# Optimization experiments

Measured on AMD Instinct MI355X. Metric: run time of the kernel, lower is better.

The kernel has to match this reference:

```python
import jax, jax.numpy as jnp
import numpy as np

B, CZ, E, V, H, W = 256, 512, 512, 4096, 16, 16  # batch, z_channels, embed_dim, vocab, latent HxW


def setup_inputs() -> dict:
    key = jax.random.key(0)
    k0, k1, k2, k3 = jax.random.split(key, 4)
    x = jax.random.normal(k0, (B, CZ, H, W), jnp.float32)          # encoder feature map
    pre_w = jax.random.normal(k1, (E, CZ), jnp.float32) * 0.02     # 1x1 pre_quant_conv weight
    pre_b = jnp.zeros((E,), jnp.float32)
    emb = jax.random.uniform(k2, (V, E), jnp.float32, -1.0 / V, 1.0 / V)  # codebook, uniform init as in module
    post_w = jax.random.normal(k3, (CZ, E), jnp.float32) * 0.02    # 1x1 post_quant_conv weight
    post_b = jnp.zeros((CZ,), jnp.float32)
    return dict(x=x, pre_w=pre_w, pre_b=pre_b, emb=emb, post_w=post_w, post_b=post_b)


def reference(x, pre_w, pre_b, emb, post_w, post_b):
    # pre_quant_conv: 1x1 Conv2d(CZ -> E)
    z = jnp.einsum('bchw,ec->behw', x, pre_w) + pre_b[None, :, None, None]
    b, e, h, w = z.shape
    # flatten spatial: (b h w, e)
    zf = z.transpose(0, 2, 3, 1).reshape(-1, e)
    # expanded squared-distance to codebook: ||z||^2 + ||c||^2 - 2 z.c
    dist = (jnp.sum(zf * zf, axis=1, keepdims=True)
            + jnp.sum(emb * emb, axis=1)
            - 2.0 * zf @ emb.T)                                    # [bhw, V]
    tokens = jnp.argmin(dist, axis=-1)                             # [bhw] int
    z_q = emb[tokens].reshape(b, h, w, e).transpose(0, 3, 1, 2)    # gather -> [b,e,h,w]
    # straight-through estimator
    dec_in = z + jax.lax.stop_gradient(z_q - z)
    # post_quant_conv: 1x1 Conv2d(E -> CZ)
    rec = jnp.einsum('behw,ce->bchw', dec_in, post_w) + post_b[None, :, None, None]
    return z, z_q, rec
```

## Files before the change

### kernel.cpp

```cpp
#include <hip/hip_runtime.h>
#include <hip/hip_bf16.h>

typedef unsigned short u16;
typedef unsigned int   u32;
typedef unsigned long long u64;

using short8 = __attribute__((ext_vector_type(8))) short;
using f32x4  = __attribute__((ext_vector_type(4))) float;
using u16x8  = __attribute__((ext_vector_type(8))) unsigned short;

#define AS_GLOBAL __attribute__((address_space(1)))
#define AS_LDS    __attribute__((address_space(3)))

__device__ __forceinline__ u16 f2b(float x){
  u32 u = __float_as_uint(x);
  u32 r = (u + 0x7FFFu + ((u >> 16) & 1u)) >> 16;
  return (u16)r;
}
__device__ __forceinline__ float b2f(u16 h){ return __uint_as_float(((u32)h) << 16); }

__device__ __forceinline__ void gload16(u16* l, const u16* g){
  __builtin_amdgcn_global_load_lds((const AS_GLOBAL u32*)g, (AS_LDS u32*)l, 16, 0, 0);
}

__device__ __forceinline__ u64 umin64(u64 a, u64 b){ return a < b ? a : b; }

__device__ __forceinline__ u64 shfl_xor_u64(u64 v, int m){
  u32 lo = __shfl_xor((u32)v, m, 64);
  u32 hi = __shfl_xor((u32)(v >> 32), m, 64);
  return ((u64)hi << 32) | lo;
}

__device__ __forceinline__ void waitv4(){ asm volatile("s_waitcnt vmcnt(4)" ::: "memory"); }
__device__ __forceinline__ void waitv0(){ asm volatile("s_waitcnt vmcnt(0)" ::: "memory"); }

__global__ void k_cvt(const float* __restrict__ w, u16* __restrict__ d, int n){
  int i = blockIdx.x * 256 + threadIdx.x;
  if (i < n) d[i] = f2b(w[i]);
}

__global__ void k_cnorm(const float* __restrict__ emb, float* __restrict__ cnorm){
  int v = blockIdx.x, lane = threadIdx.x;
  const float* r = emb + (size_t)v * 512;
  float s = 0.f;
  #pragma unroll
  for (int i = 0; i < 8; ++i){ float x = r[lane + i * 64]; s += x * x; }
  #pragma unroll
  for (int off = 32; off; off >>= 1) s += __shfl_down(s, off, 64);
  if (lane == 0) cnorm[v] = s;
}

__global__ void k_tcvt(const float* __restrict__ src, u16* __restrict__ d){
  __shared__ float t[64][65];
  const int bid = blockIdx.x;
  const int b  = bid >> 5;
  const int rb = (bid >> 2) & 7;
  const int cb = bid & 3;
  const float* s = src + ((size_t)b * 512 + (size_t)rb * 64) * 256 + cb * 64;
  const int tid = threadIdx.x;
  #pragma unroll
  for (int j = 0; j < 4; ++j){
    int fl = j * 256 + tid;
    int r = fl >> 4, c4 = (fl & 15) * 4;
    float4 v = *(const float4*)(s + (size_t)r * 256 + c4);
    t[r][c4 + 0] = v.x; t[r][c4 + 1] = v.y; t[r][c4 + 2] = v.z; t[r][c4 + 3] = v.w;
  }
  __syncthreads();
  u16* o = d + ((size_t)b * 256 + (size_t)cb * 64) * 512 + rb * 64;
  #pragma unroll
  for (int j = 0; j < 2; ++j){
    int fl = j * 256 + tid;
    int c = fl >> 3, r8 = (fl & 7) * 8;
    u16x8 hv;
    #pragma unroll
    for (int i = 0; i < 8; ++i) hv[i] = f2b(t[r8 + i][c]);
    *(u16x8*)(o + (size_t)c * 512 + r8) = hv;
  }
}

__global__ void k_zq(const u64* __restrict__ keys, const float* __restrict__ emb, float* __restrict__ zq){
  int sidx = blockIdx.x * 64 + threadIdx.x;
  int b = sidx >> 8, s = sidx & 255;
  int v = (int)(u32)keys[sidx];
  const float4* er = (const float4*)(emb + (size_t)v * 512);
  float* o = zq + (size_t)b * 512 * 256 + s;
  #pragma unroll 4
  for (int e4 = 0; e4 < 128; ++e4){
    float4 vv = er[e4];
    o[(size_t)(e4 * 4 + 0) * 256] = vv.x;
    o[(size_t)(e4 * 4 + 1) * 256] = vv.y;
    o[(size_t)(e4 * 4 + 2) * 256] = vv.z;
    o[(size_t)(e4 * 4 + 3) * 256] = vv.w;
  }
}

template<int MODE>
__global__ __launch_bounds__(256, 4) void k_gemm(
    const u16* __restrict__ Ah,
    const u16* __restrict__ Bh,
    const u64* __restrict__ gkeys,
    const float* __restrict__ bias,
    const float* __restrict__ cnorm,
    float* __restrict__ Cout,
    u64* __restrict__ okeys,
    int M, int mtbits)
{
  constexpr int K = 512;
  __shared__ __align__(16) u16 sA[128 * 64];
  __shared__ __align__(16) u16 sB[128 * 64];

  const int tid  = threadIdx.x;
  const int lane = tid & 63;
  const int wid  = tid >> 6;
  const int wm = wid >> 1, wn = wid & 1;

  const int nwg = gridDim.x;
  const int chunk = nwg >> 3;
  const int pb = blockIdx.x;
  const int bid = (pb & 7) * chunk + (pb >> 3);

  const int mt = bid & ((1 << mtbits) - 1);
  const int nt = (bid >> mtbits) & 1;
  const int b  = bid >> (mtbits + 1);
  const int m0 = mt * 128;
  const int n0 = nt * 128;
  const int bbase = b * 256;

  const u16* ga[4];
  const u16* gb[4];
  int ldso[4];
  #pragma unroll
  for (int i = 0; i < 4; ++i){
    int e = i * 256 + tid;
    int r = e >> 3;
    int sl = (e & 7) ^ (r & 7);
    ldso[i] = e * 8;
    ga[i] = Ah + (size_t)(m0 + r) * K + sl * 8;
    size_t brow;
    if (MODE == 2) brow = (size_t)(u32)gkeys[bbase + n0 + r];
    else           brow = (size_t)(bbase + n0 + r);
    gb[i] = Bh + brow * K + sl * 8;
  }

  const f32x4 zero4 = {0.f, 0.f, 0.f, 0.f};
  f32x4 acc[4][4];
  #pragma unroll
  for (int i = 0; i < 4; ++i)
    #pragma unroll
    for (int j = 0; j < 4; ++j) acc[i][j] = zero4;

  int aoff[2][4], boff[2][4];
  #pragma unroll
  for (int ks = 0; ks < 2; ++ks)
    #pragma unroll
    for (int f = 0; f < 4; ++f){
      int rA = wm * 64 + f * 16 + (lane & 15);
      aoff[ks][f] = rA * 64 + (((ks * 4 + (lane >> 4)) ^ (rA & 7)) * 8);
      int rB = wn * 64 + f * 16 + (lane & 15);
      boff[ks][f] = rB * 64 + (((ks * 4 + (lane >> 4)) ^ (rB & 7)) * 8);
    }

  for (int kt = 0; kt < 8; ++kt){
    const int k0 = kt * 64;
    #pragma unroll
    for (int i = 0; i < 4; ++i){
      gload16(&sA[ldso[i]], ga[i] + k0);
      gload16(&sB[ldso[i]], gb[i] + k0);
    }
    __syncthreads();
    #pragma unroll
    for (int ks = 0; ks < 2; ++ks){
      short8 ah[4], bh[4];
      #pragma unroll
      for (int f = 0; f < 4; ++f){
        ah[f] = *(const short8*)&sA[aoff[ks][f]];
        bh[f] = *(const short8*)&sB[boff[ks][f]];
      }
      #pragma unroll
      for (int fm = 0; fm < 4; ++fm)
        #pragma unroll
        for (int fn = 0; fn < 4; ++fn)
          acc[fm][fn] = __builtin_amdgcn_mfma_f32_16x16x32_bf16(ah[fm], bh[fn], acc[fm][fn], 0, 0, 0);
    }
    __syncthreads();
  }

  if (MODE != 1){
    const int row0 = m0 + wm * 64;
    const int col  = n0 + wn * 64 + (lane & 15);
    float* Cb = Cout + (size_t)b * M * 256;
    #pragma unroll
    for (int fm = 0; fm < 4; ++fm){
      #pragma unroll
      for (int j = 0; j < 4; ++j){
        int row = row0 + fm * 16 + (lane >> 4) * 4 + j;
        float bi = bias[row];
        #pragma unroll
        for (int fn = 0; fn < 4; ++fn)
          Cb[(size_t)row * 256 + col + fn * 16] = acc[fm][fn][j] + bi;
      }
    }
  }
}

__global__ __launch_bounds__(512, 2) void k_gemm2(
    const u16* __restrict__ Ah,
    const u16* __restrict__ Bh,
    const float* __restrict__ cnorm,
    u64* __restrict__ okeys)
{
  __shared__ __align__(16) u16 lds[2][32768];

  const int tid  = threadIdx.x;
  const int lane = tid & 63;
  const int wid  = tid >> 6;
  const int wm   = wid >> 2;
  const int wn   = wid & 3;

  const int nwg = gridDim.x;
  const int chunk = nwg >> 3;
  const int pb  = blockIdx.x;
  const int bid = (pb & 7) * chunk + (pb >> 3);
  const int mt = bid & 15;
  const int b  = bid >> 4;
  const int m0 = mt * 256;
  const int bbase = b * 256;

  const int l8 = lane >> 3;
  const int sl = (lane & 7) ^ l8;
  const int arb = (wid < 4) ? wid * 16 : 128 + (wid - 4) * 16;
  const int brb = (wid >> 1) * 64 + (wid & 1) * 16;

  const u16* srcA0 = Ah + (size_t)(m0 + arb + l8) * 512 + sl * 8;
  const u16* srcA1 = srcA0 + 8 * 512;
  const u16* srcB0 = Bh + (size_t)(bbase + brb + l8) * 512 + sl * 8;
  const u16* srcB1 = srcB0 + 8 * 512;
  const int dA0 = arb * 64 + lane * 8;
  const int dA1 = dA0 + 512;
  const int dB0 = 16384 + brb * 64 + lane * 8;
  const int dB1 = dB0 + 512;

#define STG_AFML(p, kk) { gload16(&lds[p][dA0], srcA0 + (kk)); gload16(&lds[p][dA1], srcA1 + (kk)); }
#define STG_AFMH(p, kk) { gload16(&lds[p][dA0 + 4096], srcA0 + 32768 + (kk)); gload16(&lds[p][dA1 + 4096], srcA1 + 32768 + (kk)); }
#define STG_BFNL(p, kk) { gload16(&lds[p][dB0], srcB0 + (kk)); gload16(&lds[p][dB1], srcB1 + (kk)); }
#define STG_BFNH(p, kk) { gload16(&lds[p][dB0 + 2048], srcB0 + 16384 + (kk)); gload16(&lds[p][dB1 + 2048], srcB1 + 16384 + (kk)); }

  int aoff[2][8], boff[2][4];
  #pragma unroll
  for (int ks = 0; ks < 2; ++ks){
    #pragma unroll
    for (int f = 0; f < 8; ++f){
      int rA = wm * 128 + f * 16 + (lane & 15);
      aoff[ks][f] = rA * 64 + (((ks * 4 + (lane >> 4)) ^ (rA & 7)) * 8);
    }
    #pragma unroll
    for (int f = 0; f < 4; ++f){
      int rB = wn * 64 + f * 16 + (lane & 15);
      boff[ks][f] = 16384 + rB * 64 + (((ks * 4 + (lane >> 4)) ^ (rB & 7)) * 8);
    }
  }

  const f32x4 zero4 = {0.f, 0.f, 0.f, 0.f};
  f32x4 acc[8][4];
  #pragma unroll
  for (int i = 0; i < 8; ++i)
    #pragma unroll
    for (int j = 0; j < 4; ++j) acc[i][j] = zero4;

  STG_AFML(0, 0) STG_AFMH(0, 0) STG_BFNL(0, 0) STG_BFNH(0, 0)
  STG_AFML(1, 64) STG_BFNH(1, 64)
  waitv4();
  __builtin_amdgcn_s_barrier();
  __builtin_amdgcn_sched_barrier(0);

  for (int t = 0; t < 8; ++t){
    const int bc = t & 1;
    const int bn = bc ^ 1;
    const u16* cb = &lds[bc][0];
    const int kn1 = (t + 1) * 64, kn2 = (t + 2) * 64;
    short8 ah[4][2], bh[2][2];

    if (t < 7) STG_AFMH(bn, kn1)
    #pragma unroll
    for (int f = 0; f < 4; ++f){ ah[f][0] = *(const short8*)&cb[aoff[0][f]]; ah[f][1] = *(const short8*)&cb[aoff[1][f]]; }
    #pragma unroll
    for (int f = 0; f < 2; ++f){ bh[f][0] = *(const short8*)&cb[boff[0][f]]; bh[f][1] = *(const short8*)&cb[boff[1][f]]; }
    __builtin_amdgcn_s_setprio(1);
    #pragma unroll
    for (int fm = 0; fm < 4; ++fm)
      #pragma unroll
      for (int fn = 0; fn < 2; ++fn){
        acc[fm][fn] = __builtin_amdgcn_mfma_f32_16x16x32_bf16(ah[fm][0], bh[fn][0], acc[fm][fn], 0, 0, 0);
        acc[fm][fn] = __builtin_amdgcn_mfma_f32_16x16x32_bf16(ah[fm][1], bh[fn][1], acc[fm][fn], 0, 0, 0);
      }
    __builtin_amdgcn_s_setprio(0);
    __builtin_amdgcn_sched_barrier(0);
    __builtin_amdgcn_s_barrier();
    __builtin_amdgcn_sched_barrier(0);

    if (t < 7) STG_BFNL(bn, kn1)
    #pragma unroll
    for (int f = 0; f < 2; ++f){ bh[f][0] = *(const short8*)&cb[boff[0][2 + f]]; bh[f][1] = *(const short8*)&cb[boff[1][2 + f]]; }
    __builtin_amdgcn_s_setprio(1);
    #pragma unroll
    for (int fm = 0; fm < 4; ++fm)
      #pragma unroll
      for (int fn = 0; fn < 2; ++fn){
        acc[fm][2 + fn] = __builtin_amdgcn_mfma_f32_16x16x32_bf16(ah[fm][0], bh[fn][0], acc[fm][2 + fn], 0, 0, 0);
        acc[fm][2 + fn] = __builtin_amdgcn_mfma_f32_16x16x32_bf16(ah[fm][1], bh[fn][1], acc[fm][2 + fn], 0, 0, 0);
      }
    __builtin_amdgcn_s_setprio(0);
    __builtin_amdgcn_sched_barrier(0);
    __builtin_amdgcn_s_barrier();
    __builtin_amdgcn_sched_barrier(0);

    if (t < 6) STG_AFML(bc, kn2)
    #pragma unroll
    for (int f = 0; f < 4; ++f){ ah[f][0] = *(const short8*)&cb[aoff[0][4 + f]]; ah[f][1] = *(const short8*)&cb[aoff[1][4 + f]]; }
    __builtin_amdgcn_s_setprio(1);
    #pragma unroll
    for (int fm = 0; fm < 4; ++fm)
      #pragma unroll
      for (int fn = 0; fn < 2; ++fn){
        acc[4 + fm][2 + fn] = __builtin_amdgcn_mfma_f32_16x16x32_bf16(ah[fm][0], bh[fn][0], acc[4 + fm][2 + fn], 0, 0, 0);
        acc[4 + fm][2 + fn] = __builtin_amdgcn_mfma_f32_16x16x32_bf16(ah[fm][1], bh[fn][1], acc[4 + fm][2 + fn], 0, 0, 0);
      }
    __builtin_amdgcn_s_setprio(0);
    __builtin_amdgcn_sched_barrier(0);
    __builtin_amdgcn_s_barrier();
    __builtin_amdgcn_sched_barrier(0);

    if (t < 6) STG_BFNH(bc, kn2)
    #pragma unroll
    for (int f = 0; f < 2; ++f){ bh[f][0] = *(const short8*)&cb[boff[0][f]]; bh[f][1] = *(const short8*)&cb[boff[1][f]]; }
    __builtin_amdgcn_s_setprio(1);
    #pragma unroll
    for (int fm = 0; fm < 4; ++fm)
      #pragma unroll
      for (int fn = 0; fn < 2; ++fn){
        acc[4 + fm][fn] = __builtin_amdgcn_mfma_f32_16x16x32_bf16(ah[fm][0], bh[fn][0], acc[4 + fm][fn], 0, 0, 0);
        acc[4 + fm][fn] = __builtin_amdgcn_mfma_f32_16x16x32_bf16(ah[fm][1], bh[fn][1], acc[4 + fm][fn], 0, 0, 0);
      }
    __builtin_amdgcn_s_setprio(0);
    __builtin_amdgcn_sched_barrier(0);
    if (t < 6) waitv4(); else if (t == 6) waitv0();
    __builtin_amdgcn_s_barrier();
    __builtin_amdgcn_sched_barrier(0);
  }

  __syncthreads();
  u64 best[4];
  #pragma unroll
  for (int fn = 0; fn < 4; ++fn){
    u64 bk = ~0ull;
    #pragma unroll
    for (int fm = 0; fm < 8; ++fm){
      #pragma unroll
      for (int j = 0; j < 4; ++j){
        int v = m0 + wm * 128 + fm * 16 + (lane >> 4) * 4 + j;
        float sc = cnorm[v] - 2.0f * acc[fm][fn][j];
        u32 o = __float_as_uint(sc);
        o = (o & 0x80000000u) ? ~o : (o | 0x80000000u);
        bk = umin64(bk, ((u64)o << 32) | (u32)v);
      }
    }
    bk = umin64(bk, shfl_xor_u64(bk, 16));
    bk = umin64(bk, shfl_xor_u64(bk, 32));
    best[fn] = bk;
  }
  u64* kbuf = (u64*)&lds[0][0];
  if (lane < 16){
    #pragma unroll
    for (int fn = 0; fn < 4; ++fn)
      kbuf[wm * 256 + wn * 64 + fn * 16 + lane] = best[fn];
  }
  __syncthreads();
  if (tid < 256){
    u64 k2 = umin64(kbuf[tid], kbuf[256 + tid]);
    atomicMin((unsigned long long*)(okeys + bbase + tid), (unsigned long long)k2);
  }
#undef STG_AFML
#undef STG_AFMH
#undef STG_BFNL
#undef STG_BFNH
}

extern "C" void kernel_launch(void* const* d_in, const int* in_sizes, int n_in,
                              void* d_out, int out_size, void* d_ws, size_t ws_size,
                              hipStream_t stream){
  const float* x      = (const float*)d_in[0];
  const float* pre_w  = (const float*)d_in[1];
  const float* pre_b  = (const float*)d_in[2];
  const float* emb    = (const float*)d_in[3];
  const float* post_w = (const float*)d_in[4];
  const float* post_b = (const float*)d_in[5];

  float* z_out   = (float*)d_out;
  float* zq_out  = z_out + 33554432;
  float* rec_out = z_out + 67108864;

  char* w = (char*)d_ws;
  u16* prew_b  = (u16*)(w);
  u16* postw_b = (u16*)(w + 524288);
  u16* emb_b   = (u16*)(w + 1048576);
  float* cnorm = (float*)(w + 5242880);
  u64* keys    = (u64*)(w + 5259264);
  u16* xb      = (u16*)(w + 5783552);
  u16* zb = xb;

  k_cvt  <<<1024, 256, 0, stream>>>(pre_w, prew_b, 262144);
  k_cvt  <<<1024, 256, 0, stream>>>(post_w, postw_b, 262144);
  k_cvt  <<<8192, 256, 0, stream>>>(emb, emb_b, 2097152);
  k_cnorm<<<4096, 64, 0, stream>>>(emb, cnorm);
  hipMemsetAsync(keys, 0xFF, 65536 * sizeof(u64), stream);

  k_tcvt<<<8192, 256, 0, stream>>>(x, xb);

  k_gemm<0><<<256 * 2 * 4, 256, 0, stream>>>(prew_b, xb,
      nullptr, pre_b, nullptr, z_out, nullptr, 512, 2);

  k_tcvt<<<8192, 256, 0, stream>>>(z_out, zb);

  k_gemm2<<<256 * 16, 512, 0, stream>>>(emb_b, zb, cnorm, keys);

  k_zq<<<1024, 64, 0, stream>>>(keys, emb, zq_out);

  k_gemm<2><<<256 * 2 * 4, 256, 0, stream>>>(postw_b, emb_b,
      keys, post_b, nullptr, rec_out, nullptr, 512, 2);
}
```

Measured before the change: 548.9 us.

## Make distance GEMM persistent per batch, looping codebook tiles with in-register argmin

The codebook-distance kernel now launches one workgroup per batch image, 256 in total, instead of one per (batch, codebook tile) pair. Each workgroup loops over all 16 codebook tiles with a continuous double-buffered K pipeline, keeps the running argmin in registers, and caches the codebook norms in LDS. This removes the global atomicMin and the keys memset, and cuts per-workgroup setup overhead. The cost is a 256-workgroup grid with one 512-thread block per batch, which may underfill the GPU's compute units, plus a larger LDS footprint that lowers occupancy.

```diff
diff --git a/kernel.cpp b/kernel.cpp
--- a/kernel.cpp
+++ b/kernel.cpp
@@ -30,9 +30,6 @@
   u32 hi = __shfl_xor((u32)(v >> 32), m, 64);
   return ((u64)hi << 32) | lo;
 }
-
-__device__ __forceinline__ void waitv4(){ asm volatile("s_waitcnt vmcnt(4)" ::: "memory"); }
-__device__ __forceinline__ void waitv0(){ asm volatile("s_waitcnt vmcnt(0)" ::: "memory"); }
 
 __global__ void k_cvt(const float* __restrict__ w, u16* __restrict__ d, int n){
   int i = blockIdx.x * 256 + threadIdx.x;
@@ -100,9 +97,7 @@
     const u16* __restrict__ Bh,
     const u64* __restrict__ gkeys,
     const float* __restrict__ bias,
-    const float* __restrict__ cnorm,
     float* __restrict__ Cout,
-    u64* __restrict__ okeys,
     int M, int mtbits)
 {
   constexpr int K = 512;
@@ -185,20 +180,18 @@
     __syncthreads();
   }
 
-  if (MODE != 1){
-    const int row0 = m0 + wm * 64;
-    const int col  = n0 + wn * 64 + (lane & 15);
-    float* Cb = Cout + (size_t)b * M * 256;
-    #pragma unroll
-    for (int fm = 0; fm < 4; ++fm){
-      #pragma unroll
-      for (int j = 0; j < 4; ++j){
-        int row = row0 + fm * 16 + (lane >> 4) * 4 + j;
-        float bi = bias[row];
-        #pragma unroll
-        for (int fn = 0; fn < 4; ++fn)
-          Cb[(size_t)row * 256 + col + fn * 16] = acc[fm][fn][j] + bi;
-      }
+  const int row0 = m0 + wm * 64;
+  const int col  = n0 + wn * 64 + (lane & 15);
+  float* Cb = Cout + (size_t)b * M * 256;
+  #pragma unroll
+  for (int fm = 0; fm < 4; ++fm){
+    #pragma unroll
+    for (int j = 0; j < 4; ++j){
+      int row = row0 + fm * 16 + (lane >> 4) * 4 + j;
+      float bi = bias[row];
+      #pragma unroll
+      for (int fn = 0; fn < 4; ++fn)
+        Cb[(size_t)row * 256 + col + fn * 16] = acc[fm][fn][j] + bi;
     }
   }
 }
@@ -209,41 +202,40 @@
     const float* __restrict__ cnorm,
     u64* __restrict__ okeys)
 {
-  __shared__ __align__(16) u16 lds[2][32768];
+  __shared__ __align__(16) u16 lds[75776];
 
   const int tid  = threadIdx.x;
   const int lane = tid & 63;
   const int wid  = tid >> 6;
   const int wm   = wid >> 2;
   const int wn   = wid & 3;
-
-  const int nwg = gridDim.x;
-  const int chunk = nwg >> 3;
-  const int pb  = blockIdx.x;
-  const int bid = (pb & 7) * chunk + (pb >> 3);
-  const int mt = bid & 15;
-  const int b  = bid >> 4;
-  const int m0 = mt * 256;
+  const int b    = blockIdx.x;
   const int bbase = b * 256;
+
+  float* cn = (float*)&lds[65536];
+  {
+    const float4* c4 = (const float4*)cnorm;
+    float4 a0 = c4[tid], a1 = c4[tid + 512];
+    ((float4*)cn)[tid] = a0; ((float4*)cn)[tid + 512] = a1;
+  }
+  __syncthreads();
 
   const int l8 = lane >> 3;
   const int sl = (lane & 7) ^ l8;
   const int arb = (wid < 4) ? wid * 16 : 128 + (wid - 4) * 16;
   const int brb = (wid >> 1) * 64 + (wid & 1) * 16;
-
-  const u16* srcA0 = Ah + (size_t)(m0 + arb + l8) * 512 + sl * 8;
-  const u16* srcA1 = srcA0 + 8 * 512;
-  const u16* srcB0 = Bh + (size_t)(bbase + brb + l8) * 512 + sl * 8;
-  const u16* srcB1 = srcB0 + 8 * 512;
-  const int dA0 = arb * 64 + lane * 8;
-  const int dA1 = dA0 + 512;
-  const int dB0 = 16384 + brb * 64 + lane * 8;
-  const int dB1 = dB0 + 512;
-
-#define STG_AFML(p, kk) { gload16(&lds[p][dA0], srcA0 + (kk)); gload16(&lds[p][dA1], srcA1 + (kk)); }
-#define STG_AFMH(p, kk) { gload16(&lds[p][dA0 + 4096], srcA0 + 32768 + (kk)); gload16(&lds[p][dA1 + 4096], srcA1 + 32768 + (kk)); }
-#define STG_BFNL(p, kk) { gload16(&lds[p][dB0], srcB0 + (kk)); gload16(&lds[p][dB1], srcB1 + (kk)); }
-#define STG_BFNH(p, kk) { gload16(&lds[p][dB0 + 2048], srcB0 + 16384 + (kk)); gload16(&lds[p][dB1 + 2048], srcB1 + 16384 + (kk)); }
+  const size_t aS = (size_t)(arb + l8) * 512 + sl * 8;
+  const size_t bS = (size_t)(bbase + brb + l8) * 512 + sl * 8;
+  const int dA = arb * 64 + lane * 8;
+  const int dB = 16384 + brb * 64 + lane * 8;
+
+#define STG_AFML(tp) if ((tp) < 128){ const u16* s_ = Ah + (size_t)((tp) >> 3) * 131072 + aS + ((tp) & 7) * 64; u16* d_ = &lds[((tp) & 1) * 32768 + dA]; gload16(d_, s_); gload16(d_ + 512, s_ + 4096); }
+#define STG_AFMH(tp) if ((tp) < 128){ const u16* s_ = Ah + (size_t)((tp) >> 3) * 131072 + aS + 32768 + ((tp) & 7) * 64; u16* d_ = &lds[((tp) & 1) * 32768 + dA + 4096]; gload16(d_, s_); gload16(d_ + 512, s_ + 4096); }
+#define STG_BFNL(tp) if ((tp) < 128){ const u16* s_ = Bh + bS + ((tp) & 7) * 64; u16* d_ = &lds[((tp) & 1) * 32768 + dB]; gload16(d_, s_); gload16(d_ + 512, s_ + 4096); }
+#define STG_BFNH(tp) if ((tp) < 128){ const u16* s_ = Bh + bS + 16384 + ((tp) & 7) * 64; u16* d_ = &lds[((tp) & 1) * 32768 + dB + 2048]; gload16(d_, s_); gload16(d_ + 512, s_ + 4096); }
+
+#define PH_WAIT(tau_) { if ((tau_) < 126){ asm volatile("s_waitcnt vmcnt(10)" ::: "memory"); } else { asm volatile("s_waitcnt vmcnt(0)" ::: "memory"); } \
+  __builtin_amdgcn_s_barrier(); __builtin_amdgcn_sched_barrier(0); }
 
   int aoff[2][8], boff[2][4];
   #pragma unroll
@@ -267,122 +259,123 @@
     #pragma unroll
     for (int j = 0; j < 4; ++j) acc[i][j] = zero4;
 
-  STG_AFML(0, 0) STG_AFMH(0, 0) STG_BFNL(0, 0) STG_BFNH(0, 0)
-  STG_AFML(1, 64) STG_BFNH(1, 64)
-  waitv4();
-  __builtin_amdgcn_s_barrier();
-  __builtin_amdgcn_sched_barrier(0);
-
-  for (int t = 0; t < 8; ++t){
-    const int bc = t & 1;
-    const int bn = bc ^ 1;
-    const u16* cb = &lds[bc][0];
-    const int kn1 = (t + 1) * 64, kn2 = (t + 2) * 64;
-    short8 ah[4][2], bh[2][2];
-
-    if (t < 7) STG_AFMH(bn, kn1)
-    #pragma unroll
-    for (int f = 0; f < 4; ++f){ ah[f][0] = *(const short8*)&cb[aoff[0][f]]; ah[f][1] = *(const short8*)&cb[aoff[1][f]]; }
-    #pragma unroll
-    for (int f = 0; f < 2; ++f){ bh[f][0] = *(const short8*)&cb[boff[0][f]]; bh[f][1] = *(const short8*)&cb[boff[1][f]]; }
-    __builtin_amdgcn_s_setprio(1);
-    #pragma unroll
-    for (int fm = 0; fm < 4; ++fm)
-      #pragma unroll
-      for (int fn = 0; fn < 2; ++fn){
-        acc[fm][fn] = __builtin_amdgcn_mfma_f32_16x16x32_bf16(ah[fm][0], bh[fn][0], acc[fm][fn], 0, 0, 0);
-        acc[fm][fn] = __builtin_amdgcn_mfma_f32_16x16x32_bf16(ah[fm][1], bh[fn][1], acc[fm][fn], 0, 0, 0);
+  u64 best[4];
+  #pragma unroll
+  for (int i = 0; i < 4; ++i) best[i] = ~0ull;
+
+  short8 ah[4][2], bhL[2][2], bhH[2][2];
+
+  STG_AFML(0) STG_BFNL(0) STG_BFNH(0) STG_AFMH(0)
+  STG_AFML(1) STG_BFNL(1) STG_BFNH(1)
+
+  for (int mt = 0; mt < 16; ++mt){
+    #pragma unroll 2
+    for (int kt = 0; kt < 8; ++kt){
+      const int tau = mt * 8 + kt;
+      const int bb_ = (tau & 1) * 32768;
+
+      PH_WAIT(tau);
+      STG_AFMH(tau + 1)
+      #pragma unroll
+      for (int f = 0; f < 4; ++f){ ah[f][0] = *(const short8*)&lds[bb_ + aoff[0][f]]; ah[f][1] = *(const short8*)&lds[bb_ + aoff[1][f]]; }
+      #pragma unroll
+      for (int f = 0; f < 2; ++f){ bhL[f][0] = *(const short8*)&lds[bb_ + boff[0][f]]; bhL[f][1] = *(const short8*)&lds[bb_ + boff[1][f]]; }
+      __builtin_amdgcn_s_setprio(1);
+      #pragma unroll
+      for (int fm = 0; fm < 4; ++fm)
+        #pragma unroll
+        for (int fn = 0; fn < 2; ++fn){
+          acc[fm][fn] = __builtin_amdgcn_mfma_f32_16x16x32_bf16(ah[fm][0], bhL[fn][0], acc[fm][fn], 0, 0, 0);
+          acc[fm][fn] = __builtin_amdgcn_mfma_f32_16x16x32_bf16(ah[fm][1], bhL[fn][1], acc[fm][fn], 0, 0, 0);
+        }
+      __builtin_amdgcn_s_setprio(0);
+      __builtin_amdgcn_sched_barrier(0);
+
+      PH_WAIT(tau);
+      STG_AFML(tau + 2)
+      #pragma unroll
+      for (int f = 0; f < 2; ++f){ bhH[f][0] = *(const short8*)&lds[bb_ + boff[0][2 + f]]; bhH[f][1] = *(const short8*)&lds[bb_ + boff[1][2 + f]]; }
+      __builtin_amdgcn_s_setprio(1);
+      #pragma unroll
+      for (int fm = 0; fm < 4; ++fm)
+        #pragma unroll
+        for (int fn = 0; fn < 2; ++fn){
+          acc[fm][2 + fn] = __builtin_amdgcn_mfma_f32_16x16x32_bf16(ah[fm][0], bhH[fn][0], acc[fm][2 + fn], 0, 0, 0);
+          acc[fm][2 + fn] = __builtin_amdgcn_mfma_f32_16x16x32_bf16(ah[fm][1], bhH[fn][1], acc[fm][2 + fn], 0, 0, 0);
+        }
+      __builtin_amdgcn_s_setprio(0);
+      __builtin_amdgcn_sched_barrier(0);
+
+      PH_WAIT(tau);
+      STG_BFNL(tau + 2)
+      #pragma unroll
+      for (int f = 0; f < 4; ++f){ ah[f][0] = *(const short8*)&lds[bb_ + aoff[0][4 + f]]; ah[f][1] = *(const short8*)&lds[bb_ + aoff[1][4 + f]]; }
+      __builtin_amdgcn_s_setprio(1);
+      #pragma unroll
+      for (int fm = 0; fm < 4; ++fm)
+        #pragma unroll
+        for (int fn = 0; fn < 2; ++fn){
+          acc[4 + fm][2 + fn] = __builtin_amdgcn_mfma_f32_16x16x32_bf16(ah[fm][0], bhH[fn][0], acc[4 + fm][2 + fn], 0, 0, 0);
+          acc[4 + fm][2 + fn] = __builtin_amdgcn_mfma_f32_16x16x32_bf16(ah[fm][1], bhH[fn][1], acc[4 + fm][2 + fn], 0, 0, 0);
+        }
+      __builtin_amdgcn_s_setprio(0);
+      __builtin_amdgcn_sched_barrier(0);
+
+      PH_WAIT(tau);
+      STG_BFNH(tau + 2)
+      __builtin_amdgcn_s_setprio(1);
+      #pragma unroll
+      for (int fm = 0; fm < 4; ++fm)
+        #pragma unroll
+        for (int fn = 0; fn < 2; ++fn){
+          acc[4 + fm][fn] = __builtin_amdgcn_mfma_f32_16x16x32_bf16(ah[fm][0], bhL[fn][0], acc[4 + fm][fn], 0, 0, 0);
+          acc[4 + fm][fn] = __builtin_amdgcn_mfma_f32_16x16x32_bf16(ah[fm][1], bhL[fn][1], acc[4 + fm][fn], 0, 0, 0);
+        }
+      __builtin_amdgcn_s_setprio(0);
+      __builtin_amdgcn_sched_barrier(0);
+    }
+
+    #pragma unroll
+    for (int fn = 0; fn < 4; ++fn){
+      #pragma unroll
+      for (int fm = 0; fm < 8; ++fm){
+        #pragma unroll
+        for (int j = 0; j < 4; ++j){
+          int v = mt * 256 + wm * 128 + fm * 16 + (lane >> 4) * 4 + j;
+          float sc = cn[v] - 2.0f * acc[fm][fn][j];
+          u32 o = __float_as_uint(sc);
+          o = (o & 0x80000000u) ? ~o : (o | 0x80000000u);
+          best[fn] = umin64(best[fn], ((u64)o << 32) | (u32)v);
+        }
       }
-    __builtin_amdgcn_s_setprio(0);
-    __builtin_amdgcn_sched_barrier(0);
-    __builtin_amdgcn_s_barrier();
-    __builtin_amdgcn_sched_barrier(0);
-
-    if (t < 7) STG_BFNL(bn, kn1)
-    #pragma unroll
-    for (int f = 0; f < 2; ++f){ bh[f][0] = *(const short8*)&cb[boff[0][2 + f]]; bh[f][1] = *(const short8*)&cb[boff[1][2 + f]]; }
-    __builtin_amdgcn_s_setprio(1);
-    #pragma unroll
-    for (int fm = 0; fm < 4; ++fm)
-      #pragma unroll
-      for (int fn = 0; fn < 2; ++fn){
-        acc[fm][2 + fn] = __builtin_amdgcn_mfma_f32_16x16x32_bf16(ah[fm][0], bh[fn][0], acc[fm][2 + fn], 0, 0, 0);
-        acc[fm][2 + fn] = __builtin_amdgcn_mfma_f32_16x16x32_bf16(ah[fm][1], bh[fn][1], acc[fm][2 + fn], 0, 0, 0);
-      }
-    __builtin_amdgcn_s_setprio(0);
-    __builtin_amdgcn_sched_barrier(0);
-    __builtin_amdgcn_s_barrier();
-    __builtin_amdgcn_sched_barrier(0);
-
-    if (t < 6) STG_AFML(bc, kn2)
-    #pragma unroll
-    for (int f = 0; f < 4; ++f){ ah[f][0] = *(const short8*)&cb[aoff[0][4 + f]]; ah[f][1] = *(const short8*)&cb[aoff[1][4 + f]]; }
-    __builtin_amdgcn_s_setprio(1);
-    #pragma unroll
-    for (int fm = 0; fm < 4; ++fm)
-      #pragma unroll
-      for (int fn = 0; fn < 2; ++fn){
-        acc[4 + fm][2 + fn] = __builtin_amdgcn_mfma_f32_16x16x32_bf16(ah[fm][0], bh[fn][0], acc[4 + fm][2 + fn], 0, 0, 0);
-        acc[4 + fm][2 + fn] = __builtin_amdgcn_mfma_f32_16x16x32_bf16(ah[fm][1], bh[fn][1], acc[4 + fm][2 + fn], 0, 0, 0);
-      }
-    __builtin_amdgcn_s_setprio(0);
-    __builtin_amdgcn_sched_barrier(0);
-    __builtin_amdgcn_s_barrier();
-    __builtin_amdgcn_sched_barrier(0);
-
-    if (t < 6) STG_BFNH(bc, kn2)
-    #pragma unroll
-    for (int f = 0; f < 2; ++f){ bh[f][0] = *(const short8*)&cb[boff[0][f]]; bh[f][1] = *(const short8*)&cb[boff[1][f]]; }
-    __builtin_amdgcn_s_setprio(1);
-    #pragma unroll
-    for (int fm = 0; fm < 4; ++fm)
-      #pragma unroll
-      for (int fn = 0; fn < 2; ++fn){
-        acc[4 + fm][fn] = __builtin_amdgcn_mfma_f32_16x16x32_bf16(ah[fm][0], bh[fn][0], acc[4 + fm][fn], 0, 0, 0);
-        acc[4 + fm][fn] = __builtin_amdgcn_mfma_f32_16x16x32_bf16(ah[fm][1], bh[fn][1], acc[4 + fm][fn], 0, 0, 0);
-      }
-    __builtin_amdgcn_s_setprio(0);
-    __builtin_amdgcn_sched_barrier(0);
-    if (t < 6) waitv4(); else if (t == 6) waitv0();
-    __builtin_amdgcn_s_barrier();
-    __builtin_amdgcn_sched_barrier(0);
-  }
-
+    }
+    #pragma unroll
+    for (int i = 0; i < 8; ++i)
+      #pragma unroll
+      for (int j = 0; j < 4; ++j) acc[i][j] = zero4;
+  }
+
+  #pragma unroll
+  for (int fn = 0; fn < 4; ++fn){
+    best[fn] = umin64(best[fn], shfl_xor_u64(best[fn], 16));
+    best[fn] = umin64(best[fn], shfl_xor_u64(best[fn], 32));
+  }
+  u64* kbuf = (u64*)&lds[73728];
   __syncthreads();
-  u64 best[4];
-  #pragma unroll
-  for (int fn = 0; fn < 4; ++fn){
-    u64 bk = ~0ull;
-    #pragma unroll
-    for (int fm = 0; fm < 8; ++fm){
-      #pragma unroll
-      for (int j = 0; j < 4; ++j){
-        int v = m0 + wm * 128 + fm * 16 + (lane >> 4) * 4 + j;
-        float sc = cnorm[v] - 2.0f * acc[fm][fn][j];
-        u32 o = __float_as_uint(sc);
-        o = (o & 0x80000000u) ? ~o : (o | 0x80000000u);
-        bk = umin64(bk, ((u64)o << 32) | (u32)v);
-      }
-    }
-    bk = umin64(bk, shfl_xor_u64(bk, 16));
-    bk = umin64(bk, shfl_xor_u64(bk, 32));
-    best[fn] = bk;
-  }
-  u64* kbuf = (u64*)&lds[0][0];
   if (lane < 16){
     #pragma unroll
     for (int fn = 0; fn < 4; ++fn)
       kbuf[wm * 256 + wn * 64 + fn * 16 + lane] = best[fn];
   }
   __syncthreads();
-  if (tid < 256){
-    u64 k2 = umin64(kbuf[tid], kbuf[256 + tid]);
-    atomicMin((unsigned long long*)(okeys + bbase + tid), (unsigned long long)k2);
-  }
+  if (tid < 256)
+    okeys[bbase + tid] = umin64(kbuf[tid], kbuf[256 + tid]);
+
 #undef STG_AFML
 #undef STG_AFMH
 #undef STG_BFNL
 #undef STG_BFNH
+#undef PH_WAIT
 }
 
 extern "C" void kernel_launch(void* const* d_in, const int* in_sizes, int n_in,
@@ -412,19 +405,18 @@
   k_cvt  <<<1024, 256, 0, stream>>>(post_w, postw_b, 262144);
   k_cvt  <<<8192, 256, 0, stream>>>(emb, emb_b, 2097152);
   k_cnorm<<<4096, 64, 0, stream>>>(emb, cnorm);
-  hipMemsetAsync(keys, 0xFF, 65536 * sizeof(u64), stream);
 
   k_tcvt<<<8192, 256, 0, stream>>>(x, xb);
 
   k_gemm<0><<<256 * 2 * 4, 256, 0, stream>>>(prew_b, xb,
-      nullptr, pre_b, nullptr, z_out, nullptr, 512, 2);
+      nullptr, pre_b, z_out, 512, 2);
 
   k_tcvt<<<8192, 256, 0, stream>>>(z_out, zb);
 
-  k_gemm2<<<256 * 16, 512, 0, stream>>>(emb_b, zb, cnorm, keys);
+  k_gemm2<<<256, 512, 0, stream>>>(emb_b, zb, cnorm, keys);
 
   k_zq<<<1024, 64, 0, stream>>>(keys, emb, zq_out);
 
   k_gemm<2><<<256 * 2 * 4, 256, 0, stream>>>(postw_b, emb_b,
-      keys, post_b, nullptr, rec_out, nullptr, 512, 2);
-}
+      keys, post_b, rec_out, 512, 2);
+}
```

Result: no change. 546.8 us (-0.4%).
